# Performance work log

Measured on AMD Instinct MI355X. Metric: run time of the kernel, lower is better.

## Reference

```python
import jax, jax.numpy as jnp
import numpy as np

ORDER = 63
CODEBOOK_SIZE = 256
MIN_DATA = 1
N_ITER = 5
EPS = 1e-05
PERTURB = 1e-05


def setup_inputs() -> dict:
    key = jax.random.key(0)
    x = jax.random.normal(key, (131072, ORDER + 1), dtype=jnp.float32)
    return {"x": x}


def _e_step(x, cb, T):
    # squared euclidean distances via gram trick: (T, curr)
    d2 = jnp.sum(x * x, 1)[:, None] - 2.0 * (x @ cb.T) + jnp.sum(cb * cb, 1)[None, :]
    idx = jnp.argmin(d2, axis=1)
    xq = cb[idx]
    dist = jnp.sum((x - xq) ** 2) / T
    return idx, dist


def _m_step(x, idx, curr, key):
    D = x.shape[1]
    ones = jnp.ones((x.shape[0],), x.dtype)
    n_data = jax.ops.segment_sum(ones, idx, num_segments=curr)        # histc
    mask = n_data >= MIN_DATA
    sums = jax.ops.segment_sum(x, idx, num_segments=curr)             # scatter_add
    cent = sums / jnp.maximum(n_data, 1.0)[:, None]
    m = jnp.argmax(n_data)
    r = jax.random.normal(key, (curr, D), x.dtype) * PERTURB
    nm = (~mask).astype(x.dtype)
    # empty clusters reseeded from the largest cluster, perturbed
    new = jnp.where(mask[:, None], cent, cent[m][None, :] - r)
    cnt = jnp.sum(nm)
    corr = jnp.sum(r * nm[:, None], axis=0) / jnp.maximum(cnt, 1.0)
    new = new.at[m].add(jnp.where(cnt > 0, corr, jnp.zeros_like(corr)))
    return new


def _lbg(x):
    T, D = x.shape
    K = CODEBOOK_SIZE
    codebook = jnp.full((K, D), 1e10, x.dtype).at[0].set(jnp.mean(x, axis=0))
    distance = jnp.asarray(jnp.inf, x.dtype)
    base = jax.random.key(42)
    curr = 1
    split = 0
    while curr * 2 <= K:  # static loop over log2(K) binary splits
        key_s = jax.random.fold_in(base, split)
        kr, kloop = jax.random.split(key_s)
        r = jax.random.normal(kr, (curr, D), x.dtype) * PERTURB
        codebook = codebook.at[curr:2 * curr].set(codebook[:curr] - r).at[:curr].add(r)
        curr *= 2
        prev = distance

        def body(carry, n, curr=curr):
            cb, prev_d, dist, done, key = carry
            idx, d_new = _e_step(x, cb, T)
            change = jnp.abs(prev_d - d_new)
            conv = (n > 0) & (change / (d_new + 1e-16) < EPS)
            key, sub = jax.random.split(key)
            cb_new = _m_step(x, idx, curr, sub)
            stop = done | conv
            cb_out = jnp.where(stop, cb, cb_new)        # skip m-step on convergence/break
            dist_out = jnp.where(done, dist, d_new)     # distance assigned before break
            prev_out = jnp.where(stop, prev_d, d_new)
            return (cb_out, prev_out, dist_out, stop, key), None

        carry0 = (codebook[:curr], prev, distance, jnp.asarray(False), kloop)
        (cb_fin, _, distance, _, _), _ = jax.lax.scan(body, carry0, jnp.arange(N_ITER))
        codebook = codebook.at[:curr].set(cb_fin)
        split += 1
    return codebook, distance


def reference(x):
    return _lbg(x)
```

## Files before the change

kernel.cpp:

```cpp
#include <hip/hip_runtime.h>
#include <stdint.h>


#define NPTS 131072
#define DIMS 64
#define KCB  256

struct LbgState { float dist; float prev; unsigned int done; unsigned int k0, k1; unsigned int pad; };

__device__ __forceinline__ uint32_t rotl32(uint32_t v, int n){ return (v<<n)|(v>>(32-n)); }

__device__ __forceinline__ void tf2x32(uint32_t k0, uint32_t k1, uint32_t x0, uint32_t x1,
                                       uint32_t& o0, uint32_t& o1){
  uint32_t ks2 = k0 ^ k1 ^ 0x1BD11BDAu;
  x0 += k0; x1 += k1;
  #define TFR(r) { x0 += x1; x1 = rotl32(x1, r); x1 ^= x0; }
  TFR(13) TFR(15) TFR(26) TFR(6)
  x0 += k1; x1 += ks2 + 1u;
  TFR(17) TFR(29) TFR(16) TFR(24)
  x0 += ks2; x1 += k0 + 2u;
  TFR(13) TFR(15) TFR(26) TFR(6)
  x0 += k0; x1 += k1 + 3u;
  TFR(17) TFR(29) TFR(16) TFR(24)
  x0 += k1; x1 += ks2 + 4u;
  TFR(13) TFR(15) TFR(26) TFR(6)
  x0 += ks2; x1 += k0 + 5u;
  #undef TFR
  o0 = x0; o1 = x1;
}

__device__ __forceinline__ float xla_erfinv_f32(float x){
  float w = -log1pf(-x*x);
  float p;
  if (w < 5.0f){
    w = w - 2.5f;
    p = 2.81022636e-08f;
    p = fmaf(p, w, 3.43273939e-07f);
    p = fmaf(p, w, -3.5233877e-06f);
    p = fmaf(p, w, -4.39150654e-06f);
    p = fmaf(p, w, 0.00021858087f);
    p = fmaf(p, w, -0.00125372503f);
    p = fmaf(p, w, -0.00417768164f);
    p = fmaf(p, w, 0.246640727f);
    p = fmaf(p, w, 1.50140941f);
  } else {
    w = sqrtf(w) - 3.0f;
    p = -0.000200214257f;
    p = fmaf(p, w, 0.000100950558f);
    p = fmaf(p, w, 0.00134934322f);
    p = fmaf(p, w, -0.00367342844f);
    p = fmaf(p, w, 0.00573950773f);
    p = fmaf(p, w, -0.0076224613f);
    p = fmaf(p, w, 0.00943887047f);
    p = fmaf(p, w, 1.00167406f);
    p = fmaf(p, w, 2.83297682f);
  }
  return p * x;
}

__device__ __forceinline__ float jax_normal_elem(uint32_t k0, uint32_t k1, uint32_t j){
  uint32_t o0, o1; tf2x32(k0, k1, 0u, j, o0, o1);
  uint32_t bits = o0 ^ o1;
  uint32_t fb = (bits >> 9) | 0x3f800000u;
  float f = __uint_as_float(fb) - 1.0f;
  const float lo = -0.99999994f;
  float u = f * 2.0f + lo;
  u = fmaxf(lo, u);
  return 1.41421356f * xla_erfinv_f32(u);
}

__device__ void do_split(float* __restrict__ cb, float* __restrict__ cnorm,
                         unsigned long long* __restrict__ sums,
                         unsigned int* __restrict__ ndata,
                         unsigned long long* __restrict__ distacc,
                         LbgState* __restrict__ st, int curr, int split, int t){
  __shared__ uint32_t kr0s, kr1s;
  if (t == 0){
    uint32_t ks0, ks1, a0, a1, b0, b1;
    tf2x32(0u, 42u, 0u, (uint32_t)split, ks0, ks1);
    tf2x32(ks0, ks1, 0u, 0u, a0, a1);
    tf2x32(ks0, ks1, 0u, 1u, b0, b1);
    kr0s = a0; kr1s = a1;
    st->k0 = b0; st->k1 = b1;
    st->prev = st->dist;
    st->done = 0u;
  }
  __syncthreads();
  const int n = curr * DIMS;
  for (int e = t; e < n; e += 256){
    int c = e >> 6, d = e & 63;
    float rv = jax_normal_elem(kr0s, kr1s, (uint32_t)e) * 1e-5f;
    float old = cb[c*DIMS + d];
    cb[(curr + c)*DIMS + d] = old - rv;
    cb[c*DIMS + d]          = old + rv;
  }
  __syncthreads();
  const int c2 = curr * 2;
  for (int c = t; c < c2; c += 256){
    float s = 0.f;
    for (int d = 0; d < DIMS; d++){ float vv = cb[c*DIMS+d]; s += vv*vv; }
    cnorm[c] = s;
  }
  for (int e = t; e < c2*DIMS; e += 256) sums[e] = 0ull;
  for (int c = t; c < c2; c += 256) ndata[c] = 0u;
  if (t == 0) *distacc = 0ull;
}

__global__ void mean_kernel(const float* __restrict__ x, unsigned long long* __restrict__ macc,
                            float* __restrict__ cb, float* __restrict__ cnorm,
                            unsigned long long* __restrict__ sums,
                            unsigned int* __restrict__ ndata,
                            unsigned long long* __restrict__ distacc,
                            LbgState* __restrict__ st, unsigned int* __restrict__ mcnt){
  __shared__ double part[256];
  __shared__ float stage[16*64];
  __shared__ int islast;
  const int t = threadIdx.x;
  const int d = t & 63;
  const int w = t >> 6;
  const size_t base = (size_t)blockIdx.x * 1024;
  const int lrow = t >> 4;
  const int lcol = (t & 15) * 4;

  const float4* xg = reinterpret_cast<const float4*>(x);
  float4 nxt = xg[((base + lrow) * DIMS + lcol) >> 2];
  double s = 0.0;
  for (int tt = 0; tt < 64; tt++){
    float4 cur = nxt;
    if (tt < 63)
      nxt = xg[((base + (tt+1)*16 + lrow) * DIMS + lcol) >> 2];
    __syncthreads();
    *reinterpret_cast<float4*>(&stage[lrow*DIMS + lcol]) = cur;
    __syncthreads();
    s += (double)stage[(w    )*DIMS + d];
    s += (double)stage[(w + 4)*DIMS + d];
    s += (double)stage[(w + 8)*DIMS + d];
    s += (double)stage[(w +12)*DIMS + d];
  }
  part[t] = s;
  __syncthreads();
  if (t < 64){
    double tot = part[t] + part[64+t] + part[128+t] + part[192+t];
    atomicAdd(&macc[t], (unsigned long long)__double2ll_rn(tot * 1099511627776.0));
  }
  __threadfence();
  __syncthreads();
  if (t == 0) islast = (atomicAdd(mcnt, 1u) == (unsigned)(gridDim.x - 1));
  __syncthreads();
  if (!islast) return;

  if (t < 64){
    long long mv = (long long)atomicAdd(&macc[t], 0ull);
    double mean = (double)mv * (1.0/1099511627776.0) / 131072.0;
    cb[t] = (float)mean;
  }
  for (int e = t; e < KCB*DIMS; e += 256)
    if (e >= 64) cb[e] = 1e10f;
  if (t == 0){
    st->dist = __builtin_inff();
    st->prev = __builtin_inff();
    st->done = 0u;
    atomicExch(mcnt, 0u);
  }
  __syncthreads();
  do_split(cb, cnorm, sums, ndata, distacc, st, 1, 0, t);
}

template<int CURR>
__global__ __launch_bounds__(256, 4)
void estep_kernel(const float* __restrict__ x, const float* __restrict__ cb,
                  const float* __restrict__ cnorm, unsigned char* __restrict__ bidx8,
                  unsigned long long* __restrict__ distacc, const LbgState* __restrict__ st){
  if (st->done) return;
  const int t = threadIdx.x;
  const int lane = t & 63;
  const int p = blockIdx.x * 256 + t;

  float xv[DIMS];
  const float4* xp = reinterpret_cast<const float4*>(x + (size_t)p * DIMS);
  #pragma unroll
  for (int i = 0; i < 16; i++){
    float4 v = xp[i];
    xv[4*i+0] = v.x; xv[4*i+1] = v.y; xv[4*i+2] = v.z; xv[4*i+3] = v.w;
  }
  float xx = 0.f;
  #pragma unroll
  for (int d = 0; d < DIMS; d++) xx += xv[d] * xv[d];

  constexpr int NJ = (CURR < 4) ? CURR : 4;
  float best = __builtin_inff();
  int bi = 0;
  for (int j0 = 0; j0 < CURR; j0 += NJ){
    const float* crow = cb + (size_t)j0 * DIMS;
    float acc[NJ];
    #pragma unroll
    for (int k = 0; k < NJ; k++) acc[k] = 0.f;
    #pragma unroll
    for (int d = 0; d < DIMS; d++){
      #pragma unroll
      for (int k = 0; k < NJ; k++)
        acc[k] = fmaf(xv[d], crow[k*DIMS + d], acc[k]);
    }
    #pragma unroll
    for (int k = 0; k < NJ; k++){
      float d2 = (xx - 2.0f*acc[k]) + cnorm[j0 + k];
      if (d2 < best){ best = d2; bi = j0 + k; }
    }
  }
  bidx8[p] = (unsigned char)bi;

  double dd = 0.0;
  const float4* cbv = reinterpret_cast<const float4*>(cb + (size_t)bi * DIMS);
  #pragma unroll
  for (int i = 0; i < 16; i++){
    float4 b = cbv[i];
    float df, sq;
    df = xv[4*i+0] - b.x; sq = df*df; dd += (double)sq;
    df = xv[4*i+1] - b.y; sq = df*df; dd += (double)sq;
    df = xv[4*i+2] - b.z; sq = df*df; dd += (double)sq;
    df = xv[4*i+3] - b.w; sq = df*df; dd += (double)sq;
  }
  for (int off = 32; off > 0; off >>= 1) dd += __shfl_down(dd, off);
  if (lane == 0)
    atomicAdd(distacc, (unsigned long long)__double2ll_rn(dd * 4294967296.0));
}

template<int CURR>
__global__ __launch_bounds__(256, 3)
void estep_gemm(const float* __restrict__ x, const float* __restrict__ cb,
                const float* __restrict__ cnorm, unsigned char* __restrict__ bidx8,
                unsigned long long* __restrict__ distacc, const LbgState* __restrict__ st){
  if (st->done) return;
  constexpr int NPANEL = CURR / 64;
  __shared__ float4 xs[16*128];
  __shared__ float4 cbs[64*16];
  __shared__ float sxx[128];
  __shared__ unsigned char sbidx[128];
  const int t = threadIdx.x;
  const int pbase = blockIdx.x * 128;

  {
    const int p = t & 127, h = t >> 7;
    const float4* xg = reinterpret_cast<const float4*>(x) + (size_t)(pbase + p) * 16 + h * 8;
    #pragma unroll
    for (int j = 0; j < 8; j++)
      xs[(h*8 + j)*128 + p] = xg[j];
  }
  __syncthreads();
  if (t < 128){
    float xx = 0.f;
    #pragma unroll
    for (int k4 = 0; k4 < 16; k4++){
      float4 v = xs[k4*128 + t];
      xx = fmaf(v.x, v.x, xx); xx = fmaf(v.y, v.y, xx);
      xx = fmaf(v.z, v.z, xx); xx = fmaf(v.w, v.w, xx);
    }
    sxx[t] = xx;
  }
  __syncthreads();

  const int cg = t & 7;
  const int pg = t >> 3;
  float best[4] = {__builtin_inff(), __builtin_inff(), __builtin_inff(), __builtin_inff()};
  int bidx[4] = {0,0,0,0};
  float xxv[4];
  #pragma unroll
  for (int j = 0; j < 4; j++) xxv[j] = sxx[pg + 32*j];

  const float4* cbg = reinterpret_cast<const float4*>(cb);
  for (int panel = 0; panel < NPANEL; panel++){
    __syncthreads();
    for (int idx = t; idx < 1024; idx += 256){
      const int cl = idx >> 4, kk = idx & 15;
      cbs[cl*16 + (kk ^ (cl >> 3))] = cbg[(size_t)(panel*64 + cl)*16 + kk];
    }
    __syncthreads();

    const int c0 = panel*64 + cg*8;
    float acc[4][8];
    #pragma unroll
    for (int j = 0; j < 4; j++)
      #pragma unroll
      for (int cj = 0; cj < 8; cj++) acc[j][cj] = 0.f;

    for (int k4 = 0; k4 < 16; k4++){
      float4 xf[4];
      #pragma unroll
      for (int j = 0; j < 4; j++) xf[j] = xs[k4*128 + pg + 32*j];
      #pragma unroll
      for (int cj = 0; cj < 8; cj++){
        float4 cf = cbs[(cg*8 + cj)*16 + (k4 ^ cg)];
        #pragma unroll
        for (int j = 0; j < 4; j++){
          acc[j][cj] = fmaf(xf[j].x, cf.x, acc[j][cj]);
          acc[j][cj] = fmaf(xf[j].y, cf.y, acc[j][cj]);
          acc[j][cj] = fmaf(xf[j].z, cf.z, acc[j][cj]);
          acc[j][cj] = fmaf(xf[j].w, cf.w, acc[j][cj]);
        }
      }
    }
    #pragma unroll
    for (int cj = 0; cj < 8; cj++){
      float cn = cnorm[c0 + cj];
      #pragma unroll
      for (int j = 0; j < 4; j++){
        float d2 = (xxv[j] - 2.0f*acc[j][cj]) + cn;
        if (d2 < best[j]){ best[j] = d2; bidx[j] = c0 + cj; }
      }
    }
  }
  #pragma unroll
  for (int m = 1; m < 8; m <<= 1){
    #pragma unroll
    for (int j = 0; j < 4; j++){
      float ob = __shfl_xor(best[j], m, 64);
      int   oc = __shfl_xor(bidx[j], m, 64);
      if (ob < best[j] || (ob == best[j] && oc < bidx[j])){ best[j] = ob; bidx[j] = oc; }
    }
  }
  if (cg == 0){
    #pragma unroll
    for (int j = 0; j < 4; j++) sbidx[pg + 32*j] = (unsigned char)bidx[j];
  }
  __syncthreads();
  if (t < 128){
    const int bi = (int)sbidx[t];
    bidx8[pbase + t] = (unsigned char)bi;
    const float4* cbv = cbg + (size_t)bi * 16;
    double dd = 0.0;
    #pragma unroll
    for (int k4 = 0; k4 < 16; k4++){
      float4 xv = xs[k4*128 + t];
      float4 b = cbv[k4];
      float df, sq;
      df = xv.x - b.x; sq = df*df; dd += (double)sq;
      df = xv.y - b.y; sq = df*df; dd += (double)sq;
      df = xv.z - b.z; sq = df*df; dd += (double)sq;
      df = xv.w - b.w; sq = df*df; dd += (double)sq;
    }
    for (int off = 32; off > 0; off >>= 1) dd += __shfl_down(dd, off);
    if ((t & 63) == 0)
      atomicAdd(distacc, (unsigned long long)__double2ll_rn(dd * 4294967296.0));
  }
}

template<int CURR>
__global__ __launch_bounds__(256, 2)
void estep_gemm8(const float* __restrict__ x, const float* __restrict__ cb,
                 const float* __restrict__ cnorm, unsigned char* __restrict__ bidx8,
                 unsigned long long* __restrict__ distacc, const LbgState* __restrict__ st){
  if (st->done) return;
  constexpr int NPANEL = CURR / 128;
  __shared__ float4 xs[16*128];
  __shared__ float4 cbs[128*16];
  __shared__ float sxx[128];
  __shared__ unsigned char sbidx[128];
  const int t = threadIdx.x;
  const int pbase = blockIdx.x * 128;

  {
    const int p = t & 127, h = t >> 7;
    const float4* xg = reinterpret_cast<const float4*>(x) + (size_t)(pbase + p) * 16 + h * 8;
    #pragma unroll
    for (int j = 0; j < 8; j++)
      xs[(h*8 + j)*128 + p] = xg[j];
  }
  __syncthreads();
  if (t < 128){
    float xx = 0.f;
    #pragma unroll
    for (int k4 = 0; k4 < 16; k4++){
      float4 v = xs[k4*128 + t];
      xx = fmaf(v.x, v.x, xx); xx = fmaf(v.y, v.y, xx);
      xx = fmaf(v.z, v.z, xx); xx = fmaf(v.w, v.w, xx);
    }
    sxx[t] = xx;
  }
  __syncthreads();

  const int cg = t & 15;
  const int pg = t >> 4;
  float best[8], xxv[8];
  int bidx[8];
  #pragma unroll
  for (int j = 0; j < 8; j++){ best[j] = __builtin_inff(); bidx[j] = 0; xxv[j] = sxx[pg + 16*j]; }

  const float4* cbg = reinterpret_cast<const float4*>(cb);
  for (int panel = 0; panel < NPANEL; panel++){
    __syncthreads();
    for (int idx = t; idx < 2048; idx += 256){
      const int cl = idx >> 4, kk = idx & 15;
      cbs[cl*16 + (kk ^ (cl >> 3))] = cbg[(size_t)(panel*128 + cl)*16 + kk];
    }
    __syncthreads();

    const int c0 = panel*128 + cg*8;
    float acc[8][8];
    #pragma unroll
    for (int j = 0; j < 8; j++)
      #pragma unroll
      for (int cj = 0; cj < 8; cj++) acc[j][cj] = 0.f;

    for (int k4 = 0; k4 < 16; k4++){
      float4 xf[8];
      #pragma unroll
      for (int j = 0; j < 8; j++) xf[j] = xs[k4*128 + pg + 16*j];
      #pragma unroll
      for (int cj = 0; cj < 8; cj++){
        float4 cf = cbs[(cg*8 + cj)*16 + (k4 ^ cg)];
        #pragma unroll
        for (int j = 0; j < 8; j++){
          acc[j][cj] = fmaf(xf[j].x, cf.x, acc[j][cj]);
          acc[j][cj] = fmaf(xf[j].y, cf.y, acc[j][cj]);
          acc[j][cj] = fmaf(xf[j].z, cf.z, acc[j][cj]);
          acc[j][cj] = fmaf(xf[j].w, cf.w, acc[j][cj]);
        }
      }
    }
    #pragma unroll
    for (int cj = 0; cj < 8; cj++){
      float cn = cnorm[c0 + cj];
      #pragma unroll
      for (int j = 0; j < 8; j++){
        float d2 = (xxv[j] - 2.0f*acc[j][cj]) + cn;
        if (d2 < best[j]){ best[j] = d2; bidx[j] = c0 + cj; }
      }
    }
  }
  #pragma unroll
  for (int m = 1; m < 16; m <<= 1){
    #pragma unroll
    for (int j = 0; j < 8; j++){
      float ob = __shfl_xor(best[j], m, 64);
      int   oc = __shfl_xor(bidx[j], m, 64);
      if (ob < best[j] || (ob == best[j] && oc < bidx[j])){ best[j] = ob; bidx[j] = oc; }
    }
  }
  if (cg == 0){
    #pragma unroll
    for (int j = 0; j < 8; j++) sbidx[pg + 16*j] = (unsigned char)bidx[j];
  }
  __syncthreads();
  if (t < 128){
    const int bi = (int)sbidx[t];
    bidx8[pbase + t] = (unsigned char)bi;
    const float4* cbv = cbg + (size_t)bi * 16;
    double dd = 0.0;
    #pragma unroll
    for (int k4 = 0; k4 < 16; k4++){
      float4 xv = xs[k4*128 + t];
      float4 b = cbv[k4];
      float df, sq;
      df = xv.x - b.x; sq = df*df; dd += (double)sq;
      df = xv.y - b.y; sq = df*df; dd += (double)sq;
      df = xv.z - b.z; sq = df*df; dd += (double)sq;
      df = xv.w - b.w; sq = df*df; dd += (double)sq;
    }
    for (int off = 32; off > 0; off >>= 1) dd += __shfl_down(dd, off);
    if ((t & 63) == 0)
      atomicAdd(distacc, (unsigned long long)__double2ll_rn(dd * 4294967296.0));
  }
}

template<int CURR, int NBLK>
__global__ __launch_bounds__(256)
void gather_kernel(const float* __restrict__ x, const unsigned char* __restrict__ bidx8,
                   unsigned long long* __restrict__ sums, unsigned int* __restrict__ ndata,
                   const LbgState* __restrict__ st){
  if (st->done) return;
  constexpr int CLOG = __builtin_ctz(CURR);
  constexpr int NCHUNK = NBLK / CURR;
  constexpr int PPC = NPTS / NCHUNK;
  constexpr int NPW = PPC / 4;
  __shared__ long long sacc[4*64];
  __shared__ unsigned int scw[4];
  const int t = threadIdx.x;
  const int lane = t & 63;
  const int w = t >> 6;
  const int c = blockIdx.x & (CURR - 1);
  const int chunk = blockIdx.x >> CLOG;
  const int pbase = chunk * PPC + w * NPW;

  long long acc = 0;
  unsigned int cnt = 0;
  int q0 = 0, q1 = 0, q2 = 0, q3 = 0, qn = 0;
  const uint32_t* bp = reinterpret_cast<const uint32_t*>(bidx8 + pbase);
  for (int i = 0; i < NPW; i += 256){
    const uint32_t b4 = bp[(i >> 2) + lane];
    #pragma unroll
    for (int s = 0; s < 4; s++){
      unsigned long long m = __ballot(((b4 >> (8*s)) & 255u) == (unsigned)c);
      cnt += (unsigned int)__popcll(m);
      while (m){
        const int bit = __builtin_ctzll(m);
        m &= m - 1ull;
        const int p = pbase + i + bit*4 + s;
        if      (qn == 0) q0 = p;
        else if (qn == 1) q1 = p;
        else if (qn == 2) q2 = p;
        else              q3 = p;
        qn++;
        if (qn == 4){
          const float v0 = x[(size_t)q0 * DIMS + lane];
          const float v1 = x[(size_t)q1 * DIMS + lane];
          const float v2 = x[(size_t)q2 * DIMS + lane];
          const float v3 = x[(size_t)q3 * DIMS + lane];
          acc += (long long)__double2int_rn((double)v0 * 1048576.0);
          acc += (long long)__double2int_rn((double)v1 * 1048576.0);
          acc += (long long)__double2int_rn((double)v2 * 1048576.0);
          acc += (long long)__double2int_rn((double)v3 * 1048576.0);
          qn = 0;
        }
      }
    }
  }
  if (qn > 0){
    const int i1 = (qn > 1) ? q1 : q0;
    const int i2 = (qn > 2) ? q2 : q0;
    const float v0 = x[(size_t)q0 * DIMS + lane];
    const float v1 = x[(size_t)i1 * DIMS + lane];
    const float v2 = x[(size_t)i2 * DIMS + lane];
    acc += (long long)__double2int_rn((double)v0 * 1048576.0);
    if (qn > 1) acc += (long long)__double2int_rn((double)v1 * 1048576.0);
    if (qn > 2) acc += (long long)__double2int_rn((double)v2 * 1048576.0);
  }
  sacc[w*64 + lane] = acc;
  if (lane == 0) scw[w] = cnt;
  __syncthreads();
  if (w == 0){
    long long tot = sacc[lane] + sacc[64+lane] + sacc[128+lane] + sacc[192+lane];
    if (tot) atomicAdd(&sums[c*DIMS + lane], (unsigned long long)(tot * 1048576ll));
    if (lane == 0){
      unsigned int ct = scw[0] + scw[1] + scw[2] + scw[3];
      if (ct) atomicAdd(&ndata[c], ct);
    }
  }
}

__global__ void control_kernel(float* __restrict__ cb, float* __restrict__ cnorm,
                               unsigned long long* __restrict__ sums,
                               unsigned int* __restrict__ ndata,
                               unsigned long long* __restrict__ distacc,
                               LbgState* __restrict__ st, int curr, int n_iter,
                               int next_split){
  __shared__ int s_stop;
  __shared__ unsigned int sdone;
  __shared__ uint32_t sub0, sub1;
  __shared__ float cm[64];
  __shared__ int redv[256];
  __shared__ int redi[256];
  __shared__ int s_m, s_cnt;
  const int t = threadIdx.x;
  if (t == 0) sdone = st->done;
  __syncthreads();
  const unsigned int done0 = sdone;

  if (!done0){
    if (t == 0){
      double dd = (double)(long long)(*distacc) * (1.0/4294967296.0);
      float sf = (float)dd;
      float d_new = sf / 131072.0f;
      float change = fabsf(st->prev - d_new);
      int conv = (n_iter > 0) && (change / (d_new + 1e-16f) < 1e-5f);
      st->dist = d_new;
      if (!conv) st->prev = d_new;
      st->done = conv ? 1u : 0u;
      s_stop = conv;
      if (!conv){
        uint32_t a0, a1, b0, b1;
        tf2x32(st->k0, st->k1, 0u, 0u, a0, a1);
        tf2x32(st->k0, st->k1, 0u, 1u, b0, b1);
        st->k0 = a0; st->k1 = a1;
        sub0 = b0; sub1 = b1;
      }
    }
    __syncthreads();
    if (!s_stop){
      int v = (t < curr) ? (int)ndata[t] : -1;
      redv[t] = v; redi[t] = t;
      __syncthreads();
      for (int s = 128; s > 0; s >>= 1){
        if (t < s){
          if (redv[t+s] > redv[t] || (redv[t+s] == redv[t] && redi[t+s] < redi[t])){
            redv[t] = redv[t+s]; redi[t] = redi[t+s];
          }
        }
        __syncthreads();
      }
      if (t == 0) s_m = redi[0];
      __syncthreads();
      redv[t] = (t < curr && ndata[t] == 0u) ? 1 : 0;
      __syncthreads();
      for (int s = 128; s > 0; s >>= 1){
        if (t < s) redv[t] += redv[t+s];
        __syncthreads();
      }
      if (t == 0) s_cnt = redv[0];
      __syncthreads();
      const int m = s_m;
      const int cntE = s_cnt;

      if (t < 64){
        unsigned int nm_ = ndata[m]; if (nm_ < 1u) nm_ = 1u;
        double cd = (double)(long long)sums[m*DIMS + t] * (1.0/1099511627776.0) / (double)nm_;
        cm[t] = (float)cd;
      }
      __syncthreads();

      const int total = curr * DIMS;
      for (int e = t; e < total; e += 256){
        int c = e >> 6, d = e & 63;
        if (c == m) continue;
        float nv;
        unsigned int nd = ndata[c];
        if (nd >= 1u){
          double cd = (double)(long long)sums[e] * (1.0/1099511627776.0) / (double)nd;
          nv = (float)cd;
        } else {
          float rv = jax_normal_elem(sub0, sub1, (uint32_t)e) * 1e-5f;
          nv = cm[d] - rv;
        }
        cb[e] = nv;
      }
      if (t < 64){
        float add = 0.f;
        if (cntE > 0){
          float acc = 0.f;
          for (int c = 0; c < curr; c++){
            if (ndata[c] == 0u)
              acc += jax_normal_elem(sub0, sub1, (uint32_t)(c*DIMS + t)) * 1e-5f;
          }
          add = acc / fmaxf((float)cntE, 1.0f);
        }
        cb[m*DIMS + t] = cm[t] + add;
      }
      __syncthreads();

      for (int c = t; c < curr; c += 256){
        float s = 0.f;
        for (int d = 0; d < DIMS; d++){ float vv = cb[c*DIMS+d]; s += vv*vv; }
        cnorm[c] = s;
      }
      for (int e = t; e < total; e += 256) sums[e] = 0ull;
      for (int c = t; c < curr; c += 256) ndata[c] = 0u;
      if (t == 0) *distacc = 0ull;
    }
  }
  __syncthreads();
  if (n_iter == 4){
    if (curr < 256){
      do_split(cb, cnorm, sums, ndata, distacc, st, curr, next_split, t);
    } else if (t == 0){
      cb[KCB*DIMS] = st->dist;
    }
  }
}

extern "C" void kernel_launch(void* const* d_in, const int* in_sizes, int n_in,
                              void* d_out, int out_size, void* d_ws, size_t ws_size,
                              hipStream_t stream){
  const float* x = (const float*)d_in[0];
  float* cb = (float*)d_out;
  char* ws = (char*)d_ws;
  unsigned long long* sums    = (unsigned long long*)(ws + 0);
  unsigned long long* macc    = (unsigned long long*)(ws + 131072);
  unsigned long long* distacc = (unsigned long long*)(ws + 131584);
  LbgState* st                = (LbgState*)(ws + 131592);
  unsigned int* ndata         = (unsigned int*)(ws + 131616);
  float* cnorm                = (float*)(ws + 132640);
  unsigned char* bidx8        = (unsigned char*)(ws + 133664);
  unsigned int* mcnt          = (unsigned int*)(ws + 264736);

  hipMemsetAsync(d_ws, 0, 264744, stream);
  mean_kernel<<<128, 256, 0, stream>>>(x, macc, cb, cnorm, sums, ndata, distacc, st, mcnt);

  for (int split = 0; split < 8; split++){
    const int curr = 2 << split;
    for (int n = 0; n < 5; n++){
      switch (curr){
        case 2:   estep_kernel<2>  <<<512,256,0,stream>>>(x,cb,cnorm,bidx8,distacc,st);
                  gather_kernel<2,256>   <<<256, 256,0,stream>>>(x,bidx8,sums,ndata,st); break;
        case 4:   estep_kernel<4>  <<<512,256,0,stream>>>(x,cb,cnorm,bidx8,distacc,st);
                  gather_kernel<4,512>   <<<512, 256,0,stream>>>(x,bidx8,sums,ndata,st); break;
        case 8:   estep_kernel<8>  <<<512,256,0,stream>>>(x,cb,cnorm,bidx8,distacc,st);
                  gather_kernel<8,512>   <<<512, 256,0,stream>>>(x,bidx8,sums,ndata,st); break;
        case 16:  estep_kernel<16> <<<512,256,0,stream>>>(x,cb,cnorm,bidx8,distacc,st);
                  gather_kernel<16,512>  <<<512, 256,0,stream>>>(x,bidx8,sums,ndata,st); break;
        case 32:  estep_kernel<32> <<<512,256,0,stream>>>(x,cb,cnorm,bidx8,distacc,st);
                  gather_kernel<32,512>  <<<512, 256,0,stream>>>(x,bidx8,sums,ndata,st); break;
        case 64:  estep_gemm<64>  <<<1024,256,0,stream>>>(x,cb,cnorm,bidx8,distacc,st);
                  gather_kernel<64,512>  <<<512, 256,0,stream>>>(x,bidx8,sums,ndata,st); break;
        case 128: estep_gemm8<128><<<1024,256,0,stream>>>(x,cb,cnorm,bidx8,distacc,st);
                  gather_kernel<128,1024><<<1024,256,0,stream>>>(x,bidx8,sums,ndata,st); break;
        case 256: estep_gemm8<256><<<1024,256,0,stream>>>(x,cb,cnorm,bidx8,distacc,st);
                  gather_kernel<256,2048><<<2048,256,0,stream>>>(x,bidx8,sums,ndata,st); break;
      }
      control_kernel<<<1, 256, 0, stream>>>(cb, cnorm, sums, ndata, distacc, st, curr, n, split+1);
    }
  }
}
```

Before: 3.325 ms.

## Batch eight clusters per gather block and use estep_gemm for large codebooks

Adds a gather8_kernel in which each block stages its chunk of byte cluster indices in shared memory and then handles eight clusters in turn with ballot-based selection. This cuts the block count and avoids re-reading the index array once per cluster from global memory. It also drops the 8x8 register-tiled estep_gemm8 and uses the existing estep_gemm for 128 and 256 clusters. The trade-off is fewer blocks, which lowers parallelism for the gather step, and possibly a less efficient E-step at large K.

Result: slower. 3.776 ms (+13.5%).

```diff
diff --git a/kernel.cpp b/kernel.cpp
--- a/kernel.cpp
+++ b/kernel.cpp
@@ -344,124 +344,6 @@
   }
 }
 
-template<int CURR>
-__global__ __launch_bounds__(256, 2)
-void estep_gemm8(const float* __restrict__ x, const float* __restrict__ cb,
-                 const float* __restrict__ cnorm, unsigned char* __restrict__ bidx8,
-                 unsigned long long* __restrict__ distacc, const LbgState* __restrict__ st){
-  if (st->done) return;
-  constexpr int NPANEL = CURR / 128;
-  __shared__ float4 xs[16*128];
-  __shared__ float4 cbs[128*16];
-  __shared__ float sxx[128];
-  __shared__ unsigned char sbidx[128];
-  const int t = threadIdx.x;
-  const int pbase = blockIdx.x * 128;
-
-  {
-    const int p = t & 127, h = t >> 7;
-    const float4* xg = reinterpret_cast<const float4*>(x) + (size_t)(pbase + p) * 16 + h * 8;
-    #pragma unroll
-    for (int j = 0; j < 8; j++)
-      xs[(h*8 + j)*128 + p] = xg[j];
-  }
-  __syncthreads();
-  if (t < 128){
-    float xx = 0.f;
-    #pragma unroll
-    for (int k4 = 0; k4 < 16; k4++){
-      float4 v = xs[k4*128 + t];
-      xx = fmaf(v.x, v.x, xx); xx = fmaf(v.y, v.y, xx);
-      xx = fmaf(v.z, v.z, xx); xx = fmaf(v.w, v.w, xx);
-    }
-    sxx[t] = xx;
-  }
-  __syncthreads();
-
-  const int cg = t & 15;
-  const int pg = t >> 4;
-  float best[8], xxv[8];
-  int bidx[8];
-  #pragma unroll
-  for (int j = 0; j < 8; j++){ best[j] = __builtin_inff(); bidx[j] = 0; xxv[j] = sxx[pg + 16*j]; }
-
-  const float4* cbg = reinterpret_cast<const float4*>(cb);
-  for (int panel = 0; panel < NPANEL; panel++){
-    __syncthreads();
-    for (int idx = t; idx < 2048; idx += 256){
-      const int cl = idx >> 4, kk = idx & 15;
-      cbs[cl*16 + (kk ^ (cl >> 3))] = cbg[(size_t)(panel*128 + cl)*16 + kk];
-    }
-    __syncthreads();
-
-    const int c0 = panel*128 + cg*8;
-    float acc[8][8];
-    #pragma unroll
-    for (int j = 0; j < 8; j++)
-      #pragma unroll
-      for (int cj = 0; cj < 8; cj++) acc[j][cj] = 0.f;
-
-    for (int k4 = 0; k4 < 16; k4++){
-      float4 xf[8];
-      #pragma unroll
-      for (int j = 0; j < 8; j++) xf[j] = xs[k4*128 + pg + 16*j];
-      #pragma unroll
-      for (int cj = 0; cj < 8; cj++){
-        float4 cf = cbs[(cg*8 + cj)*16 + (k4 ^ cg)];
-        #pragma unroll
-        for (int j = 0; j < 8; j++){
-          acc[j][cj] = fmaf(xf[j].x, cf.x, acc[j][cj]);
-          acc[j][cj] = fmaf(xf[j].y, cf.y, acc[j][cj]);
-          acc[j][cj] = fmaf(xf[j].z, cf.z, acc[j][cj]);
-          acc[j][cj] = fmaf(xf[j].w, cf.w, acc[j][cj]);
-        }
-      }
-    }
-    #pragma unroll
-    for (int cj = 0; cj < 8; cj++){
-      float cn = cnorm[c0 + cj];
-      #pragma unroll
-      for (int j = 0; j < 8; j++){
-        float d2 = (xxv[j] - 2.0f*acc[j][cj]) + cn;
-        if (d2 < best[j]){ best[j] = d2; bidx[j] = c0 + cj; }
-      }
-    }
-  }
-  #pragma unroll
-  for (int m = 1; m < 16; m <<= 1){
-    #pragma unroll
-    for (int j = 0; j < 8; j++){
-      float ob = __shfl_xor(best[j], m, 64);
-      int   oc = __shfl_xor(bidx[j], m, 64);
-      if (ob < best[j] || (ob == best[j] && oc < bidx[j])){ best[j] = ob; bidx[j] = oc; }
-    }
-  }
-  if (cg == 0){
-    #pragma unroll
-    for (int j = 0; j < 8; j++) sbidx[pg + 16*j] = (unsigned char)bidx[j];
-  }
-  __syncthreads();
-  if (t < 128){
-    const int bi = (int)sbidx[t];
-    bidx8[pbase + t] = (unsigned char)bi;
-    const float4* cbv = cbg + (size_t)bi * 16;
-    double dd = 0.0;
-    #pragma unroll
-    for (int k4 = 0; k4 < 16; k4++){
-      float4 xv = xs[k4*128 + t];
-      float4 b = cbv[k4];
-      float df, sq;
-      df = xv.x - b.x; sq = df*df; dd += (double)sq;
-      df = xv.y - b.y; sq = df*df; dd += (double)sq;
-      df = xv.z - b.z; sq = df*df; dd += (double)sq;
-      df = xv.w - b.w; sq = df*df; dd += (double)sq;
-    }
-    for (int off = 32; off > 0; off >>= 1) dd += __shfl_down(dd, off);
-    if ((t & 63) == 0)
-      atomicAdd(distacc, (unsigned long long)__double2ll_rn(dd * 4294967296.0));
-  }
-}
-
 template<int CURR, int NBLK>
 __global__ __launch_bounds__(256)
 void gather_kernel(const float* __restrict__ x, const unsigned char* __restrict__ bidx8,
@@ -537,6 +419,91 @@
   }
 }
 
+template<int CURR>
+__global__ __launch_bounds__(256)
+void gather8_kernel(const float* __restrict__ x, const unsigned char* __restrict__ bidx8,
+                    unsigned long long* __restrict__ sums, unsigned int* __restrict__ ndata,
+                    const LbgState* __restrict__ st){
+  if (st->done) return;
+  constexpr int G = 8;
+  constexpr int CG = CURR / G;
+  constexpr int NCHUNK = 256 / CG;
+  constexpr int PPC = NPTS / NCHUNK;
+  constexpr int NPW = PPC / 4;
+  __shared__ long long sacc[4*64];
+  __shared__ unsigned int scw[4];
+  __shared__ uint32_t bstage[PPC/4];
+  const int t = threadIdx.x;
+  const int lane = t & 63;
+  const int w = t >> 6;
+  const int cbase = (blockIdx.x % CG) * G;
+  const int chunk = blockIdx.x / CG;
+
+  const uint32_t* bg = reinterpret_cast<const uint32_t*>(bidx8) + chunk * (PPC/4);
+  for (int idx = t; idx < PPC/4; idx += 256) bstage[idx] = bg[idx];
+  __syncthreads();
+
+  const int pbase = chunk * PPC + w * NPW;
+  const int dwbase = (w * NPW) >> 2;
+  for (int g = 0; g < G; g++){
+    const int c = cbase + g;
+    long long acc = 0;
+    unsigned int cnt = 0;
+    int q0 = 0, q1 = 0, q2 = 0, q3 = 0, qn = 0;
+    for (int i = 0; i < NPW; i += 256){
+      const uint32_t b4 = bstage[dwbase + (i >> 2) + lane];
+      #pragma unroll
+      for (int s = 0; s < 4; s++){
+        unsigned long long m = __ballot(((b4 >> (8*s)) & 255u) == (unsigned)c);
+        cnt += (unsigned int)__popcll(m);
+        while (m){
+          const int bit = __builtin_ctzll(m);
+          m &= m - 1ull;
+          const int p = pbase + i + bit*4 + s;
+          if      (qn == 0) q0 = p;
+          else if (qn == 1) q1 = p;
+          else if (qn == 2) q2 = p;
+          else              q3 = p;
+          qn++;
+          if (qn == 4){
+            const float v0 = x[(size_t)q0 * DIMS + lane];
+            const float v1 = x[(size_t)q1 * DIMS + lane];
+            const float v2 = x[(size_t)q2 * DIMS + lane];
+            const float v3 = x[(size_t)q3 * DIMS + lane];
+            acc += (long long)__double2int_rn((double)v0 * 1048576.0);
+            acc += (long long)__double2int_rn((double)v1 * 1048576.0);
+            acc += (long long)__double2int_rn((double)v2 * 1048576.0);
+            acc += (long long)__double2int_rn((double)v3 * 1048576.0);
+            qn = 0;
+          }
+        }
+      }
+    }
+    if (qn > 0){
+      const int i1 = (qn > 1) ? q1 : q0;
+      const int i2 = (qn > 2) ? q2 : q0;
+      const float v0 = x[(size_t)q0 * DIMS + lane];
+      const float v1 = x[(size_t)i1 * DIMS + lane];
+      const float v2 = x[(size_t)i2 * DIMS + lane];
+      acc += (long long)__double2int_rn((double)v0 * 1048576.0);
+      if (qn > 1) acc += (long long)__double2int_rn((double)v1 * 1048576.0);
+      if (qn > 2) acc += (long long)__double2int_rn((double)v2 * 1048576.0);
+    }
+    sacc[w*64 + lane] = acc;
+    if (lane == 0) scw[w] = cnt;
+    __syncthreads();
+    if (w == 0){
+      long long tot = sacc[lane] + sacc[64+lane] + sacc[128+lane] + sacc[192+lane];
+      if (tot) atomicAdd(&sums[c*DIMS + lane], (unsigned long long)(tot * 1048576ll));
+      if (lane == 0){
+        unsigned int ct = scw[0] + scw[1] + scw[2] + scw[3];
+        if (ct) atomicAdd(&ndata[c], ct);
+      }
+    }
+    __syncthreads();
+  }
+}
+
 __global__ void control_kernel(float* __restrict__ cb, float* __restrict__ cnorm,
                                unsigned long long* __restrict__ sums,
                                unsigned int* __restrict__ ndata,
@@ -689,11 +656,11 @@
         case 32:  estep_kernel<32> <<<512,256,0,stream>>>(x,cb,cnorm,bidx8,distacc,st);
                   gather_kernel<32,512>  <<<512, 256,0,stream>>>(x,bidx8,sums,ndata,st); break;
         case 64:  estep_gemm<64>  <<<1024,256,0,stream>>>(x,cb,cnorm,bidx8,distacc,st);
-                  gather_kernel<64,512>  <<<512, 256,0,stream>>>(x,bidx8,sums,ndata,st); break;
-        case 128: estep_gemm8<128><<<1024,256,0,stream>>>(x,cb,cnorm,bidx8,distacc,st);
-                  gather_kernel<128,1024><<<1024,256,0,stream>>>(x,bidx8,sums,ndata,st); break;
-        case 256: estep_gemm8<256><<<1024,256,0,stream>>>(x,cb,cnorm,bidx8,distacc,st);
-                  gather_kernel<256,2048><<<2048,256,0,stream>>>(x,bidx8,sums,ndata,st); break;
+                  gather8_kernel<64>     <<<256, 256,0,stream>>>(x,bidx8,sums,ndata,st); break;
+        case 128: estep_gemm<128> <<<1024,256,0,stream>>>(x,cb,cnorm,bidx8,distacc,st);
+                  gather8_kernel<128>    <<<256, 256,0,stream>>>(x,bidx8,sums,ndata,st); break;
+        case 256: estep_gemm<256> <<<1024,256,0,stream>>>(x,cb,cnorm,bidx8,distacc,st);
+                  gather8_kernel<256>    <<<256, 256,0,stream>>>(x,bidx8,sums,ndata,st); break;
       }
       control_kernel<<<1, 256, 0, stream>>>(cb, cnorm, sums, ndata, distacc, st, curr, n, split+1);
     }
```
